# Kernel optimization log

Measured on AMD Instinct MI355X. Metric: run time of the kernel, lower is better.

## Reference

```python
import jax, jax.numpy as jnp
import numpy as np

SQ, B, H, D = 2048, 1, 16, 64
HIDDEN = H * D


def setup_inputs() -> dict:
    key = jax.random.key(0)
    kq, kk, kv = jax.random.split(key, 3)
    query_layer = jax.random.normal(kq, (SQ, B, H, D), dtype=jnp.float32)
    key_layer = jax.random.normal(kk, (SQ, B, H, D), dtype=jnp.float32)
    value_layer = jax.random.normal(kv, (SQ, B, H, D), dtype=jnp.float32)
    return {"query_layer": query_layer, "key_layer": key_layer, "value_layer": value_layer}


def reference(query_layer, key_layer, value_layer):
    sq, b, h, d = query_layer.shape
    sk = key_layer.shape[0]
    norm = 1.0 / jnp.sqrt(jnp.asarray(d, dtype=query_layer.dtype))
    # scores: [b, h, sq, sk]  (materialized in the original via baddbmm)
    scores = jnp.einsum('sbhd,tbhd->bhst', query_layer, key_layer) * norm
    # causal mask (tril over [sq, sk]); masked positions -> -10000.0 as in original
    causal = jnp.tril(jnp.ones((sq, sk), dtype=bool))
    scores = jnp.where(causal[None, None], scores, jnp.asarray(-10000.0, scores.dtype))
    probs = jax.nn.softmax(scores, axis=-1)
    # context: [sq, b, h, d] -> [sq, b, hidden]
    ctx = jnp.einsum('bhst,tbhd->sbhd', probs, value_layer)
    return ctx.reshape(sq, b, h * d)
```

## Files before the change

kernel.cpp:

```cpp
#include <hip/hip_runtime.h>

typedef __bf16 bf16_t;
typedef bf16_t bf16x4 __attribute__((ext_vector_type(4)));
typedef bf16_t bf16x8 __attribute__((ext_vector_type(8)));
typedef float f32x4 __attribute__((ext_vector_type(4)));
typedef float f32x16 __attribute__((ext_vector_type(16)));

namespace {
constexpr int kNH  = 16;
constexpr int kHD  = 64;
constexpr int kHID = kNH * kHD;
constexpr int kSQ  = 2048;
constexpr int kKP  = 72;
constexpr int oQ = 0;
constexpr int oK = 64 * kKP;
constexpr int kOmPitch = 68;
constexpr int kSmBytes = 71680;
constexpr int kKbElems = kNH * kSQ * kHD;
}

__global__ __launch_bounds__(256)
void prep_kernel(const float* __restrict__ Kg, const float* __restrict__ Vg,
                 bf16_t* __restrict__ Kb, bf16_t* __restrict__ Vb) {
  const int bid = blockIdx.x;
  const int tid = threadIdx.x;
  if (bid < 1024) {
    const int o    = (bid * 256 + tid) * 8;
    const int head = o >> 17;
    const int t    = (o >> 6) & 2047;
    const int d0   = o & 63;
    const float4 f0 = *(const float4*)(Kg + (size_t)t * kHID + head * kHD + d0);
    const float4 f1 = *(const float4*)(Kg + (size_t)t * kHID + head * kHD + d0 + 4);
    bf16x8 hk;
    hk[0] = (bf16_t)f0.x; hk[1] = (bf16_t)f0.y; hk[2] = (bf16_t)f0.z; hk[3] = (bf16_t)f0.w;
    hk[4] = (bf16_t)f1.x; hk[5] = (bf16_t)f1.y; hk[6] = (bf16_t)f1.z; hk[7] = (bf16_t)f1.w;
    *(bf16x8*)(Kb + o) = hk;
  } else {
    const int vb   = bid - 1024;
    const int head = vb >> 6;
    const int tile = vb & 63;
    const int lane = tid >> 2;
    const int hh   = lane >> 5;
    const int m31  = lane & 31;
    const int q    = tid & 3;
    const int db   = q >> 1, tp = q & 1;
    const int tb   = tile * 32 + 4 * hh + 16 * tp;
    const int d    = m31 + 32 * db;
    const float* src = Vg + (size_t)tb * kHID + head * kHD + d;
    bf16x8 hv;
    #pragma unroll
    for (int j = 0; j < 8; ++j)
      hv[j] = (bf16_t)src[(size_t)((j & 3) + 8 * (j >> 2)) * kHID];
    *(bf16x8*)(Vb + ((size_t)(head * 64 + tile) * 64 + lane) * 32 + (db * 16 + tp * 8)) = hv;
  }
}

__global__ __launch_bounds__(512, 2)
void fattn_kernel(const float* __restrict__ Qg, const bf16_t* __restrict__ Kb,
                  const bf16_t* __restrict__ Vb, float* __restrict__ Og) {
  __shared__ __align__(16) unsigned char smraw[kSmBytes];
  bf16_t* sm = (bf16_t*)smraw;

  const int bid  = blockIdx.x;
  const int head = bid & (kNH - 1);
  const int ip   = bid >> 4;

  const int tid  = threadIdx.x;
  const int wave = tid >> 6;
  const int lane = tid & 63;
  const int h    = lane >> 5;
  const int m31  = lane & 31;

  bf16_t* qs = sm + oQ;
  bf16_t* ks = sm + oK + wave * 32 * kKP;

  const float kQScale = 0.125f * 1.44269504088896340736f;

  const int krow = lane >> 1;
  const int kcol = (lane & 1) * 32;
  const bf16_t* kbase = Kb + (size_t)head * (kSQ * kHD) + (size_t)krow * kHD + kcol;
  const bf16_t* vbase = Vb + ((size_t)head * 64 * 64 + lane) * 32;

  for (int halfq = 0; halfq < 2; ++halfq) {
    const int mblk = halfq ? ip : (31 - ip);
    const int m0   = mblk * 64;
    const int mtk  = 2 * mblk + 1;

    __syncthreads();
    #pragma unroll
    for (int i = 0; i < 2; ++i) {
      const int idx = tid + 512 * i;
      const int row = idx >> 4;
      const int c4  = (idx & 15) * 4;
      const float4 f = *(const float4*)(Qg + (size_t)(m0 + row) * kHID + head * kHD + c4);
      bf16x4 qv;
      qv[0] = (bf16_t)(f.x * kQScale); qv[1] = (bf16_t)(f.y * kQScale);
      qv[2] = (bf16_t)(f.z * kQScale); qv[3] = (bf16_t)(f.w * kQScale);
      *(bf16x4*)(qs + row * kKP + c4) = qv;
    }
    __syncthreads();

    f32x16 Oa00, Oa10, Oa01, Oa11;
    #pragma unroll
    for (int r = 0; r < 16; ++r) { Oa00[r] = 0.f; Oa10[r] = 0.f; Oa01[r] = 0.f; Oa11[r] = 0.f; }
    float lacc0 = 0.f, lacc1 = 0.f;

    bf16x8 kreg[4];
    bf16x8 vreg[4];

    if (wave <= mtk) {
      #pragma unroll
      for (int i = 0; i < 4; ++i)
        kreg[i] = *(const bf16x8*)(kbase + (size_t)(wave * 32) * kHD + 8 * i);
      #pragma unroll
      for (int i = 0; i < 4; ++i)
        vreg[i] = *(const bf16x8*)(vbase + (size_t)wave * 2048 + 8 * i);
    }

    for (int jt = wave; jt <= mtk; jt += 8) {
      const int kv0 = jt * 32;

      #pragma unroll
      for (int i = 0; i < 4; ++i)
        *(bf16x8*)(ks + krow * kKP + kcol + 8 * i) = kreg[i];

      bf16x8 va0 = vreg[0], va1 = vreg[1], va2 = vreg[2], va3 = vreg[3];

      if (jt + 8 <= mtk) {
        const int kn = (jt + 8) * 32;
        #pragma unroll
        for (int i = 0; i < 4; ++i)
          kreg[i] = *(const bf16x8*)(kbase + (size_t)kn * kHD + 8 * i);
        #pragma unroll
        for (int i = 0; i < 4; ++i)
          vreg[i] = *(const bf16x8*)(vbase + (size_t)(jt + 8) * 2048 + 8 * i);
      }

      if (kv0 <= m0) {
        f32x16 cs;
        #pragma unroll
        for (int r = 0; r < 16; ++r) cs[r] = 0.f;
        #pragma unroll
        for (int t = 0; t < 4; ++t) {
          bf16x8 af = *(const bf16x8*)(ks + m31 * kKP + 16 * t + 8 * h);
          bf16x8 qf = *(const bf16x8*)(qs + m31 * kKP + 16 * t + 8 * h);
          cs = __builtin_amdgcn_mfma_f32_32x32x16_bf16(af, qf, cs, 0, 0, 0);
        }
        float p[16];
        if (kv0 == m0) {
          #pragma unroll
          for (int r = 0; r < 16; ++r) {
            const int kr = (r & 3) + 8 * (r >> 2) + 4 * h;
            const float e = __builtin_amdgcn_exp2f(cs[r]);
            p[r] = (kr <= m31) ? e : 0.f;
            lacc0 += p[r];
          }
        } else {
          #pragma unroll
          for (int r = 0; r < 16; ++r) { p[r] = __builtin_amdgcn_exp2f(cs[r]); lacc0 += p[r]; }
        }
        bf16x8 pb0, pb1;
        #pragma unroll
        for (int j = 0; j < 8; ++j) { pb0[j] = (bf16_t)p[j]; pb1[j] = (bf16_t)p[8 + j]; }
        Oa00 = __builtin_amdgcn_mfma_f32_32x32x16_bf16(va0, pb0, Oa00, 0, 0, 0);
        Oa10 = __builtin_amdgcn_mfma_f32_32x32x16_bf16(va2, pb0, Oa10, 0, 0, 0);
        Oa00 = __builtin_amdgcn_mfma_f32_32x32x16_bf16(va1, pb1, Oa00, 0, 0, 0);
        Oa10 = __builtin_amdgcn_mfma_f32_32x32x16_bf16(va3, pb1, Oa10, 0, 0, 0);
      }

      {
        f32x16 cs;
        #pragma unroll
        for (int r = 0; r < 16; ++r) cs[r] = 0.f;
        #pragma unroll
        for (int t = 0; t < 4; ++t) {
          bf16x8 af = *(const bf16x8*)(ks + m31 * kKP + 16 * t + 8 * h);
          bf16x8 qf = *(const bf16x8*)(qs + (32 + m31) * kKP + 16 * t + 8 * h);
          cs = __builtin_amdgcn_mfma_f32_32x32x16_bf16(af, qf, cs, 0, 0, 0);
        }
        float p[16];
        if (kv0 == m0 + 32) {
          #pragma unroll
          for (int r = 0; r < 16; ++r) {
            const int kr = (r & 3) + 8 * (r >> 2) + 4 * h;
            const float e = __builtin_amdgcn_exp2f(cs[r]);
            p[r] = (kr <= m31) ? e : 0.f;
            lacc1 += p[r];
          }
        } else {
          #pragma unroll
          for (int r = 0; r < 16; ++r) { p[r] = __builtin_amdgcn_exp2f(cs[r]); lacc1 += p[r]; }
        }
        bf16x8 pb0, pb1;
        #pragma unroll
        for (int j = 0; j < 8; ++j) { pb0[j] = (bf16_t)p[j]; pb1[j] = (bf16_t)p[8 + j]; }
        Oa01 = __builtin_amdgcn_mfma_f32_32x32x16_bf16(va0, pb0, Oa01, 0, 0, 0);
        Oa11 = __builtin_amdgcn_mfma_f32_32x32x16_bf16(va2, pb0, Oa11, 0, 0, 0);
        Oa01 = __builtin_amdgcn_mfma_f32_32x32x16_bf16(va1, pb1, Oa01, 0, 0, 0);
        Oa11 = __builtin_amdgcn_mfma_f32_32x32x16_bf16(va3, pb1, Oa11, 0, 0, 0);
      }
    }

    float* fv   = (float*)smraw;
    float* Om   = fv + wave * 32 * kOmPitch;
    float* larr = fv + 8 * 32 * kOmPitch;

    #pragma unroll
    for (int qh = 0; qh < 2; ++qh) {
      __syncthreads();
      {
        const f32x16& A0 = qh ? Oa01 : Oa00;
        const f32x16& A1 = qh ? Oa11 : Oa10;
        #pragma unroll
        for (int q = 0; q < 4; ++q) {
          f32x4 v0, v1;
          #pragma unroll
          for (int e = 0; e < 4; ++e) { v0[e] = A0[4 * q + e]; v1[e] = A1[4 * q + e]; }
          *(f32x4*)(Om + (size_t)m31 * kOmPitch + 8 * q + 4 * h)      = v0;
          *(f32x4*)(Om + (size_t)m31 * kOmPitch + 32 + 8 * q + 4 * h) = v1;
        }
        larr[wave * 64 + lane] = qh ? lacc1 : lacc0;
      }
      __syncthreads();
      {
        const int row = tid >> 4;
        const int c4  = (tid & 15) * 4;
        float l = 0.f;
        #pragma unroll
        for (int w = 0; w < 8; ++w)
          l += larr[w * 64 + row] + larr[w * 64 + 32 + row];
        const float inv = 1.f / l;
        f32x4 o;
        #pragma unroll
        for (int e = 0; e < 4; ++e) o[e] = 0.f;
        #pragma unroll
        for (int w = 0; w < 8; ++w) {
          const f32x4 a = *(const f32x4*)(fv + w * 32 * kOmPitch + (size_t)row * kOmPitch + c4);
          #pragma unroll
          for (int e = 0; e < 4; ++e) o[e] += a[e];
        }
        #pragma unroll
        for (int e = 0; e < 4; ++e) o[e] *= inv;
        *(f32x4*)(Og + (size_t)(m0 + 32 * qh + row) * kHID + head * kHD + c4) = o;
      }
    }
  }
}

extern "C" void kernel_launch(void* const* d_in, const int* in_sizes, int n_in,
                              void* d_out, int out_size, void* d_ws, size_t ws_size,
                              hipStream_t stream) {
  (void)in_sizes; (void)n_in; (void)ws_size; (void)out_size;
  const float* Q = (const float*)d_in[0];
  const float* K = (const float*)d_in[1];
  const float* V = (const float*)d_in[2];
  float* O = (float*)d_out;
  bf16_t* Kb = (bf16_t*)d_ws;
  bf16_t* Vb = Kb + kKbElems;
  hipLaunchKernelGGL(prep_kernel, dim3(2048), dim3(256), 0, stream, K, V, Kb, Vb);
  dim3 grid(256);
  dim3 block(512);
  hipLaunchKernelGGL(fattn_kernel, grid, block, 0, stream, Q, Kb, Vb, O);
}
```

Baseline: 90.39 us.

## Load K fragments directly from global into MFMA registers, cache Q fragments

Removes the per-wave K staging through shared memory: each lane now loads its K operand fragments straight from global memory in MFMA layout. Q fragments are loaded once per query block into registers instead of being re-read from LDS every tile. The prefetch is restructured into an A/B double-buffered register ping-pong. This cuts LDS traffic but raises register pressure, and the global K loads are less coalesced.

```diff
diff --git a/kernel.cpp b/kernel.cpp
--- a/kernel.cpp
+++ b/kernel.cpp
@@ -12,8 +12,6 @@
 constexpr int kHID = kNH * kHD;
 constexpr int kSQ  = 2048;
 constexpr int kKP  = 72;
-constexpr int oQ = 0;
-constexpr int oK = 64 * kKP;
 constexpr int kOmPitch = 68;
 constexpr int kSmBytes = 71680;
 constexpr int kKbElems = kNH * kSQ * kHD;
@@ -60,6 +58,7 @@
                   const bf16_t* __restrict__ Vb, float* __restrict__ Og) {
   __shared__ __align__(16) unsigned char smraw[kSmBytes];
   bf16_t* sm = (bf16_t*)smraw;
+  bf16_t* qs = sm;
 
   const int bid  = blockIdx.x;
   const int head = bid & (kNH - 1);
@@ -71,15 +70,10 @@
   const int h    = lane >> 5;
   const int m31  = lane & 31;
 
-  bf16_t* qs = sm + oQ;
-  bf16_t* ks = sm + oK + wave * 32 * kKP;
-
   const float kQScale = 0.125f * 1.44269504088896340736f;
 
-  const int krow = lane >> 1;
-  const int kcol = (lane & 1) * 32;
-  const bf16_t* kbase = Kb + (size_t)head * (kSQ * kHD) + (size_t)krow * kHD + kcol;
-  const bf16_t* vbase = Vb + ((size_t)head * 64 * 64 + lane) * 32;
+  const bf16_t* kfb = Kb + (size_t)head * (kSQ * kHD) + (size_t)m31 * kHD + 8 * h;
+  const bf16_t* vfb = Vb + ((size_t)head * 64 * 64 + lane) * 32;
 
   for (int halfq = 0; halfq < 2; ++halfq) {
     const int mblk = halfq ? ip : (31 - ip);
@@ -100,52 +94,31 @@
     }
     __syncthreads();
 
+    bf16x8 qf00 = *(const bf16x8*)(qs + m31 * kKP +  0 + 8 * h);
+    bf16x8 qf01 = *(const bf16x8*)(qs + m31 * kKP + 16 + 8 * h);
+    bf16x8 qf02 = *(const bf16x8*)(qs + m31 * kKP + 32 + 8 * h);
+    bf16x8 qf03 = *(const bf16x8*)(qs + m31 * kKP + 48 + 8 * h);
+    bf16x8 qf10 = *(const bf16x8*)(qs + (32 + m31) * kKP +  0 + 8 * h);
+    bf16x8 qf11 = *(const bf16x8*)(qs + (32 + m31) * kKP + 16 + 8 * h);
+    bf16x8 qf12 = *(const bf16x8*)(qs + (32 + m31) * kKP + 32 + 8 * h);
+    bf16x8 qf13 = *(const bf16x8*)(qs + (32 + m31) * kKP + 48 + 8 * h);
+
     f32x16 Oa00, Oa10, Oa01, Oa11;
     #pragma unroll
     for (int r = 0; r < 16; ++r) { Oa00[r] = 0.f; Oa10[r] = 0.f; Oa01[r] = 0.f; Oa11[r] = 0.f; }
     float lacc0 = 0.f, lacc1 = 0.f;
 
-    bf16x8 kreg[4];
-    bf16x8 vreg[4];
-
-    if (wave <= mtk) {
-      #pragma unroll
-      for (int i = 0; i < 4; ++i)
-        kreg[i] = *(const bf16x8*)(kbase + (size_t)(wave * 32) * kHD + 8 * i);
-      #pragma unroll
-      for (int i = 0; i < 4; ++i)
-        vreg[i] = *(const bf16x8*)(vbase + (size_t)wave * 2048 + 8 * i);
-    }
-
-    for (int jt = wave; jt <= mtk; jt += 8) {
-      const int kv0 = jt * 32;
-
-      #pragma unroll
-      for (int i = 0; i < 4; ++i)
-        *(bf16x8*)(ks + krow * kKP + kcol + 8 * i) = kreg[i];
-
-      bf16x8 va0 = vreg[0], va1 = vreg[1], va2 = vreg[2], va3 = vreg[3];
-
-      if (jt + 8 <= mtk) {
-        const int kn = (jt + 8) * 32;
-        #pragma unroll
-        for (int i = 0; i < 4; ++i)
-          kreg[i] = *(const bf16x8*)(kbase + (size_t)kn * kHD + 8 * i);
-        #pragma unroll
-        for (int i = 0; i < 4; ++i)
-          vreg[i] = *(const bf16x8*)(vbase + (size_t)(jt + 8) * 2048 + 8 * i);
-      }
-
+    auto tile = [&](bf16x8 k0, bf16x8 k1, bf16x8 k2, bf16x8 k3,
+                    bf16x8 v0, bf16x8 v1, bf16x8 v2, bf16x8 v3, int jt_) {
+      const int kv0 = jt_ * 32;
       if (kv0 <= m0) {
         f32x16 cs;
         #pragma unroll
         for (int r = 0; r < 16; ++r) cs[r] = 0.f;
-        #pragma unroll
-        for (int t = 0; t < 4; ++t) {
-          bf16x8 af = *(const bf16x8*)(ks + m31 * kKP + 16 * t + 8 * h);
-          bf16x8 qf = *(const bf16x8*)(qs + m31 * kKP + 16 * t + 8 * h);
-          cs = __builtin_amdgcn_mfma_f32_32x32x16_bf16(af, qf, cs, 0, 0, 0);
-        }
+        cs = __builtin_amdgcn_mfma_f32_32x32x16_bf16(k0, qf00, cs, 0, 0, 0);
+        cs = __builtin_amdgcn_mfma_f32_32x32x16_bf16(k1, qf01, cs, 0, 0, 0);
+        cs = __builtin_amdgcn_mfma_f32_32x32x16_bf16(k2, qf02, cs, 0, 0, 0);
+        cs = __builtin_amdgcn_mfma_f32_32x32x16_bf16(k3, qf03, cs, 0, 0, 0);
         float p[16];
         if (kv0 == m0) {
           #pragma unroll
@@ -162,22 +135,19 @@
         bf16x8 pb0, pb1;
         #pragma unroll
         for (int j = 0; j < 8; ++j) { pb0[j] = (bf16_t)p[j]; pb1[j] = (bf16_t)p[8 + j]; }
-        Oa00 = __builtin_amdgcn_mfma_f32_32x32x16_bf16(va0, pb0, Oa00, 0, 0, 0);
-        Oa10 = __builtin_amdgcn_mfma_f32_32x32x16_bf16(va2, pb0, Oa10, 0, 0, 0);
-        Oa00 = __builtin_amdgcn_mfma_f32_32x32x16_bf16(va1, pb1, Oa00, 0, 0, 0);
-        Oa10 = __builtin_amdgcn_mfma_f32_32x32x16_bf16(va3, pb1, Oa10, 0, 0, 0);
-      }
-
+        Oa00 = __builtin_amdgcn_mfma_f32_32x32x16_bf16(v0, pb0, Oa00, 0, 0, 0);
+        Oa10 = __builtin_amdgcn_mfma_f32_32x32x16_bf16(v2, pb0, Oa10, 0, 0, 0);
+        Oa00 = __builtin_amdgcn_mfma_f32_32x32x16_bf16(v1, pb1, Oa00, 0, 0, 0);
+        Oa10 = __builtin_amdgcn_mfma_f32_32x32x16_bf16(v3, pb1, Oa10, 0, 0, 0);
+      }
       {
         f32x16 cs;
         #pragma unroll
         for (int r = 0; r < 16; ++r) cs[r] = 0.f;
-        #pragma unroll
-        for (int t = 0; t < 4; ++t) {
-          bf16x8 af = *(const bf16x8*)(ks + m31 * kKP + 16 * t + 8 * h);
-          bf16x8 qf = *(const bf16x8*)(qs + (32 + m31) * kKP + 16 * t + 8 * h);
-          cs = __builtin_amdgcn_mfma_f32_32x32x16_bf16(af, qf, cs, 0, 0, 0);
-        }
+        cs = __builtin_amdgcn_mfma_f32_32x32x16_bf16(k0, qf10, cs, 0, 0, 0);
+        cs = __builtin_amdgcn_mfma_f32_32x32x16_bf16(k1, qf11, cs, 0, 0, 0);
+        cs = __builtin_amdgcn_mfma_f32_32x32x16_bf16(k2, qf12, cs, 0, 0, 0);
+        cs = __builtin_amdgcn_mfma_f32_32x32x16_bf16(k3, qf13, cs, 0, 0, 0);
         float p[16];
         if (kv0 == m0 + 32) {
           #pragma unroll
@@ -194,11 +164,46 @@
         bf16x8 pb0, pb1;
         #pragma unroll
         for (int j = 0; j < 8; ++j) { pb0[j] = (bf16_t)p[j]; pb1[j] = (bf16_t)p[8 + j]; }
-        Oa01 = __builtin_amdgcn_mfma_f32_32x32x16_bf16(va0, pb0, Oa01, 0, 0, 0);
-        Oa11 = __builtin_amdgcn_mfma_f32_32x32x16_bf16(va2, pb0, Oa11, 0, 0, 0);
-        Oa01 = __builtin_amdgcn_mfma_f32_32x32x16_bf16(va1, pb1, Oa01, 0, 0, 0);
-        Oa11 = __builtin_amdgcn_mfma_f32_32x32x16_bf16(va3, pb1, Oa11, 0, 0, 0);
-      }
+        Oa01 = __builtin_amdgcn_mfma_f32_32x32x16_bf16(v0, pb0, Oa01, 0, 0, 0);
+        Oa11 = __builtin_amdgcn_mfma_f32_32x32x16_bf16(v2, pb0, Oa11, 0, 0, 0);
+        Oa01 = __builtin_amdgcn_mfma_f32_32x32x16_bf16(v1, pb1, Oa01, 0, 0, 0);
+        Oa11 = __builtin_amdgcn_mfma_f32_32x32x16_bf16(v3, pb1, Oa11, 0, 0, 0);
+      }
+    };
+
+    bf16x8 kA0, kA1, kA2, kA3, vA0, vA1, vA2, vA3;
+    bf16x8 kB0, kB1, kB2, kB3, vB0, vB1, vB2, vB3;
+    int jt = wave;
+    if (jt <= mtk) {
+      const bf16_t* kp = kfb + (size_t)jt * 2048;
+      kA0 = *(const bf16x8*)(kp);      kA1 = *(const bf16x8*)(kp + 16);
+      kA2 = *(const bf16x8*)(kp + 32); kA3 = *(const bf16x8*)(kp + 48);
+      const bf16_t* vp = vfb + (size_t)jt * 2048;
+      vA0 = *(const bf16x8*)(vp);      vA1 = *(const bf16x8*)(vp + 8);
+      vA2 = *(const bf16x8*)(vp + 16); vA3 = *(const bf16x8*)(vp + 24);
+    }
+    while (jt <= mtk) {
+      if (jt + 8 <= mtk) {
+        const bf16_t* kp = kfb + (size_t)(jt + 8) * 2048;
+        kB0 = *(const bf16x8*)(kp);      kB1 = *(const bf16x8*)(kp + 16);
+        kB2 = *(const bf16x8*)(kp + 32); kB3 = *(const bf16x8*)(kp + 48);
+        const bf16_t* vp = vfb + (size_t)(jt + 8) * 2048;
+        vB0 = *(const bf16x8*)(vp);      vB1 = *(const bf16x8*)(vp + 8);
+        vB2 = *(const bf16x8*)(vp + 16); vB3 = *(const bf16x8*)(vp + 24);
+      }
+      tile(kA0, kA1, kA2, kA3, vA0, vA1, vA2, vA3, jt);
+      jt += 8;
+      if (jt > mtk) break;
+      if (jt + 8 <= mtk) {
+        const bf16_t* kp = kfb + (size_t)(jt + 8) * 2048;
+        kA0 = *(const bf16x8*)(kp);      kA1 = *(const bf16x8*)(kp + 16);
+        kA2 = *(const bf16x8*)(kp + 32); kA3 = *(const bf16x8*)(kp + 48);
+        const bf16_t* vp = vfb + (size_t)(jt + 8) * 2048;
+        vA0 = *(const bf16x8*)(vp);      vA1 = *(const bf16x8*)(vp + 8);
+        vA2 = *(const bf16x8*)(vp + 16); vA3 = *(const bf16x8*)(vp + 24);
+      }
+      tile(kB0, kB1, kB2, kB3, vB0, vB1, vB2, vB3, jt);
+      jt += 8;
     }
 
     float* fv   = (float*)smraw;
```

Result: slower. 120.9 us (+33.7%).
